# Kernel tuning notes

Measured on AMD Instinct MI355X. Metric: run time of the kernel, lower is better.

## Reference

```python
import jax, jax.numpy as jnp
import numpy as np

B, S, D, DS = 8, 2048, 1024, 128
TEMP = 1.0
C = 8.0


def setup_inputs() -> dict:
    key = jax.random.key(0)
    ks = jax.random.split(key, 8)
    s_in = 1.0 / np.sqrt(D)
    s_st = 1.0 / np.sqrt(DS)
    return {
        "x": jax.random.normal(ks[0], (B, S, D), jnp.float32),
        "W_k": jax.random.normal(ks[1], (DS, D), jnp.float32) * s_in,
        "W_v": jax.random.normal(ks[2], (DS, D), jnp.float32) * s_in,
        "W_q": jax.random.normal(ks[3], (DS, D), jnp.float32) * s_in,
        "W_alpha_w": jax.random.normal(ks[4], (DS, D), jnp.float32) * s_in,
        "W_alpha_b": jnp.zeros((DS,), jnp.float32),
        "lambda_param": jax.random.uniform(ks[5], (DS,), jnp.float32, 4.0, 9.0),
        "W_o": jax.random.normal(ks[6], (D, DS), jnp.float32) * s_st,
        "norm_weight": jnp.ones((DS,), jnp.float32),
    }


def _l2norm(z):
    # matches F.normalize(..., dim=-1) with eps=1e-12
    n = jnp.linalg.norm(z, axis=-1, keepdims=True)
    return z / jnp.maximum(n, 1e-12)


def reference(x, W_k, W_v, W_q, W_alpha_w, W_alpha_b, lambda_param, W_o, norm_weight):
    # projections
    k = _l2norm(x @ W_k.T)                      # [B,S,DS]
    v = x @ W_v.T                               # [B,S,DS]
    q = _l2norm(x @ W_q.T)                      # [B,S,DS]
    r = jax.nn.sigmoid(x @ W_alpha_w.T + W_alpha_b)
    log_a = jnp.log(jax.nn.sigmoid(lambda_param) + 1e-8)  # [DS]
    alpha = jnp.exp(C * r * log_a)              # [B,S,DS], data-dependent decay

    H0 = jnp.zeros((B, DS, DS), x.dtype)        # state indexed [b, k, v]

    def step(H, inp):
        k_t, v_t, q_t, a_t = inp                # each [B,DS]
        # surprise: prediction error against current state
        pred = jnp.einsum('bk,bkv->bv', q_t, H)
        err = jnp.sum((v_t - pred) ** 2, axis=-1, keepdims=True)  # [B,1]
        sur = jax.nn.sigmoid(err / (TEMP + 1e-6))                 # [B,1]
        # delta rule: k (x) v - k (x) (k^T H) = k (x) (v - k^T H)
        k_proj = jnp.einsum('bk,bkv->bv', k_t, H)
        delta = k_t[:, :, None] * (v_t - k_proj)[:, None, :]      # [B,DS,DS]
        a_e = a_t[:, :, None]                                     # decay on k-axis
        H = a_e * H + (1.0 - a_e) * (sur[:, :, None] * delta)
        y = jnp.einsum('bk,bkv->bv', q_t, H)
        return H, y

    seq = (k.transpose(1, 0, 2), v.transpose(1, 0, 2),
           q.transpose(1, 0, 2), alpha.transpose(1, 0, 2))
    _, ys = jax.lax.scan(step, H0, seq)         # ys: [S,B,DS]
    y = ys.transpose(1, 0, 2)                   # [B,S,DS]

    # RMSNorm (computed in fp32, like the torch module)
    yf = y.astype(jnp.float32)
    yn = yf * jax.lax.rsqrt(jnp.mean(yf * yf, axis=-1, keepdims=True) + 1e-6)
    yn = (yn * norm_weight).astype(y.dtype)
    return yn @ W_o.T                           # [B,S,D]
```

## Files before the change

kernel.cpp:

```cpp
#include <hip/hip_runtime.h>
#include <math.h>

#define S_LEN 2048
#define B_SZ 8
#define D_IN 1024
#define DS_ 128
#define INV_TEMP (1.0f/1.000001f)
#define LBUF 712
#define NBLK 16

#define BAR_LDS() asm volatile("s_waitcnt lgkmcnt(0)\n\ts_barrier" ::: "memory")

#define DPPADD(x, ctrl) { int t_ = __builtin_amdgcn_update_dpp( \
    0, __float_as_int(x), ctrl, 0xF, 0xF, false); x += __int_as_float(t_); }
#define ROWSUM(x) { DPPADD(x, 0x128) DPPADD(x, 0x124) DPPADD(x, 0x122) DPPADD(x, 0x121) }

__global__ __launch_bounds__(256) void proj_gemm(
    const float* __restrict__ X,
    const float* __restrict__ Wk, const float* __restrict__ Wv,
    const float* __restrict__ Wq, const float* __restrict__ Wa,
    float* __restrict__ P)
{
    __shared__ __align__(16) float As[32][68];
    __shared__ __align__(16) float Bs[32][68];
    const int tid = threadIdx.x;
    const int m0 = blockIdx.x * 64;
    const int n0 = blockIdx.y * 64;
    const int lr = tid >> 3;
    const int lk4 = tid & 7;

    const float* wrows[2];
#pragma unroll
    for (int i = 0; i < 2; i++) {
        int nn = n0 + lr + i * 32;
        const float* w;
        if      (nn < 128) w = Wk + (size_t)nn * D_IN;
        else if (nn < 256) w = Wv + (size_t)(nn - 128) * D_IN;
        else if (nn < 384) w = Wq + (size_t)(nn - 256) * D_IN;
        else               w = Wa + (size_t)(nn - 384) * D_IN;
        wrows[i] = w;
    }
    const int ty = tid >> 4, tx = tid & 15;
    float acc[4][4];
#pragma unroll
    for (int i = 0; i < 4; i++)
#pragma unroll
        for (int j = 0; j < 4; j++) acc[i][j] = 0.f;

    for (int k0 = 0; k0 < D_IN; k0 += 32) {
#pragma unroll
        for (int i = 0; i < 2; i++) {
            int m = lr + i * 32;
            float4 a4 = *(const float4*)(X + (size_t)(m0 + m) * D_IN + k0 + lk4 * 4);
            As[lk4*4+0][m] = a4.x; As[lk4*4+1][m] = a4.y;
            As[lk4*4+2][m] = a4.z; As[lk4*4+3][m] = a4.w;
            float4 b4 = *(const float4*)(wrows[i] + k0 + lk4 * 4);
            Bs[lk4*4+0][m] = b4.x; Bs[lk4*4+1][m] = b4.y;
            Bs[lk4*4+2][m] = b4.z; Bs[lk4*4+3][m] = b4.w;
        }
        __syncthreads();
#pragma unroll
        for (int kk = 0; kk < 32; kk++) {
            float4 a4 = *(const float4*)(&As[kk][ty * 4]);
            float4 b4 = *(const float4*)(&Bs[kk][tx * 4]);
            float a[4] = {a4.x, a4.y, a4.z, a4.w};
            float b[4] = {b4.x, b4.y, b4.z, b4.w};
#pragma unroll
            for (int i = 0; i < 4; i++)
#pragma unroll
                for (int j = 0; j < 4; j++)
                    acc[i][j] = fmaf(a[i], b[j], acc[i][j]);
        }
        __syncthreads();
    }
#pragma unroll
    for (int i = 0; i < 4; i++) {
        float4 o; o.x = acc[i][0]; o.y = acc[i][1]; o.z = acc[i][2]; o.w = acc[i][3];
        *(float4*)(P + (size_t)(m0 + ty * 4 + i) * 512 + n0 + tx * 4) = o;
    }
}

__global__ __launch_bounds__(128) void postproc(
    float* __restrict__ P, float* __restrict__ G,
    const float* __restrict__ bA, const float* __restrict__ lam)
{
    const int tok = blockIdx.x, i = threadIdx.x;
    float* row = P + (size_t)tok * 512;
    float kr = row[i], qr = row[256 + i], rr = row[384 + i];
    float ks = kr * kr, qs = qr * qr;
#pragma unroll
    for (int m = 1; m < 64; m <<= 1) { ks += __shfl_xor(ks, m); qs += __shfl_xor(qs, m); }
    __shared__ float sb[6];
    if ((i & 63) == 0) { sb[(i >> 6) * 2] = ks; sb[(i >> 6) * 2 + 1] = qs; }
    __syncthreads();
    float kinv = 1.0f / fmaxf(sqrtf(sb[0] + sb[2]), 1e-12f);
    float qinv = 1.0f / fmaxf(sqrtf(sb[1] + sb[3]), 1e-12f);
    float kn = kr * kinv, qn = qr * qinv;
    float sr = 1.0f / (1.0f + __expf(-(rr + bA[i])));
    float sl = 1.0f / (1.0f + __expf(-lam[i]));
    float la = logf(sl + 1e-8f);
    float al = __expf(8.0f * sr * la);
    row[i] = kn; row[256 + i] = qn; row[384 + i] = al;
    float gi = qn * (1.0f - al) * kn;
#pragma unroll
    for (int m = 1; m < 64; m <<= 1) gi += __shfl_xor(gi, m);
    if ((i & 63) == 0) sb[4 + (i >> 6)] = gi;
    __syncthreads();
    if (i == 0) G[tok] = sb[4] + sb[5];
}

__global__ __launch_bounds__(512, 2) void recurrence(
    const float* __restrict__ P, const float* __restrict__ G,
    float* __restrict__ Y, float* __restrict__ EB)
{
    const int bx = blockIdx.x;
    const int b = bx & 7;
    const int half = bx >> 3;
    const int tid = threadIdx.x;
    const int c = tid & 15;
    const int vp = tid >> 4;
    const int lane = tid & 63;
    const int wave = tid >> 6;
    const int co = c * 12;
    const int voff = 576 + half * 64 + vp * 2;

    __shared__ __align__(16) float Pbuf[3][LBUF];
    __shared__ __align__(16) float errw[2][8];

    const float* Pb = P + (size_t)b * S_LEN * 512;
    const float* Gb = G + (size_t)b * S_LEN;
    float* Yb = Y + (size_t)b * S_LEN * DS_ + half * 64;
    float* own = EB + (size_t)bx * S_LEN;
    const float* peer = EB + (size_t)(bx ^ 8) * S_LEN;

    float2 H[8];
#pragma unroll
    for (int j = 0; j < 8; j++) { H[j].x = 0.f; H[j].y = 0.f; }

    const bool isP = tid < 256;
    const bool isG = (tid == 256);
    int spos = 0;
    if (isP) {
        int i = tid * 2, s = i >> 7, idx = i & 127, cp = (idx >> 3) * 12 + (idx & 7);
        spos = (s == 0) ? cp : (s == 1) ? (576 + idx) : (s == 2) ? (192 + cp) : (384 + cp);
    }

    float2 rp0 = {0.f, 0.f}, rp1 = {0.f, 0.f};
    float rg0 = 0.f, rg1 = 0.f;
    if (isP) { rp0 = *(const float2*)(Pb + tid * 2); rp1 = *(const float2*)(Pb + 512 + tid * 2); }
    if (isG) { rg0 = Gb[0]; rg1 = Gb[1]; }
    if (isP) *(float2*)(&Pbuf[0][spos]) = rp0;
    if (isG) Pbuf[0][704] = rg0;
    __syncthreads();

    float4 k0, k1, q0, q1, a0, a1; float2 vt; float g;
#define LOADREGS(T) { float* cb = &Pbuf[(T) % 3][0]; \
    k0 = *(const float4*)(cb + co);       k1 = *(const float4*)(cb + co + 4); \
    q0 = *(const float4*)(cb + 192 + co); q1 = *(const float4*)(cb + 192 + co + 4); \
    a0 = *(const float4*)(cb + 384 + co); a1 = *(const float4*)(cb + 384 + co + 4); \
    vt = *(const float2*)(cb + voff);     g  = cb[704]; }

    LOADREGS(0)

#define STEP(T, PAR, RPS, RGS, RPL, RGL) { \
    float kk[8] = {k0.x,k0.y,k0.z,k0.w,k1.x,k1.y,k1.z,k1.w}; \
    float qq[8] = {q0.x,q0.y,q0.z,q0.w,q1.x,q1.y,q1.z,q1.w}; \
    float aa[8] = {a0.x,a0.y,a0.z,a0.w,a1.x,a1.y,a1.z,a1.w}; \
    float zz[8], ww[8]; \
    _Pragma("unroll") for (int j = 0; j < 8; j++) { \
        zz[j] = qq[j] * aa[j]; ww[j] = fmaf(-kk[j], aa[j], kk[j]); } \
    float2 pr = {0.f,0.f}, kp = {0.f,0.f}, ya = {0.f,0.f}; \
    _Pragma("unroll") for (int j = 0; j < 8; j++) { \
        pr.x = fmaf(qq[j], H[j].x, pr.x); pr.y = fmaf(qq[j], H[j].y, pr.y); \
        kp.x = fmaf(kk[j], H[j].x, kp.x); kp.y = fmaf(kk[j], H[j].y, kp.y); \
        ya.x = fmaf(zz[j], H[j].x, ya.x); ya.y = fmaf(zz[j], H[j].y, ya.y); } \
    ROWSUM(pr.x) ROWSUM(pr.y) ROWSUM(kp.x) ROWSUM(kp.y) ROWSUM(ya.x) ROWSUM(ya.y) \
    float ex = vt.x - pr.x, ey = vt.y - pr.y; \
    float ep = fmaf(ex, ex, ey * ey); \
    ep += __shfl_xor(ep, 16); ep += __shfl_xor(ep, 32); \
    if (lane == 0) errw[PAR][wave] = ep; \
    float2 d2; d2.x = vt.x - kp.x; d2.y = vt.y - kp.y; \
    const float gcur = g; const float2 yac = ya; \
    if ((T) + 1 < S_LEN) { \
        if (isP) *(float2*)(&Pbuf[((T) + 1) % 3][spos]) = RPS; \
        if (isG) Pbuf[((T) + 1) % 3][704] = RGS; } \
    if ((T) + 2 < S_LEN) { \
        if (isP) RPL = *(const float2*)(Pb + (size_t)((T) + 2) * 512 + tid * 2); \
        if (isG) RGL = Gb[(T) + 2]; } \
    BAR_LDS(); \
    const float4 ea  = *(const float4*)(&errw[PAR][0]); \
    const float4 eb2 = *(const float4*)(&errw[PAR][4]); \
    float el = ((ea.x + ea.y) + (ea.z + ea.w)) + ((eb2.x + eb2.y) + (eb2.z + eb2.w)); \
    if (tid == 0) __hip_atomic_store(own + (T), el + 1.0f, \
        __ATOMIC_RELAXED, __HIP_MEMORY_SCOPE_AGENT); \
    _Pragma("unroll") for (int j = 0; j < 8; j++) { H[j].x *= aa[j]; H[j].y *= aa[j]; } \
    if ((T) + 1 < S_LEN) LOADREGS((T) + 1) \
    float pv; \
    do { pv = __hip_atomic_load(peer + (T), \
        __ATOMIC_RELAXED, __HIP_MEMORY_SCOPE_AGENT); } while (pv == 0.0f); \
    float err = el + (pv - 1.0f); \
    float sur = 1.0f / (1.0f + __expf(-err * INV_TEMP)); \
    float2 sd; sd.x = sur * d2.x; sd.y = sur * d2.y; \
    _Pragma("unroll") for (int j = 0; j < 8; j++) { \
        H[j].x = fmaf(ww[j], sd.x, H[j].x); H[j].y = fmaf(ww[j], sd.y, H[j].y); } \
    if (c == 0) { \
        float sg = sur * gcur; float2 y2; \
        y2.x = fmaf(sg, d2.x, yac.x); y2.y = fmaf(sg, d2.y, yac.y); \
        *(float2*)(Yb + (size_t)(T) * DS_ + vp * 2) = y2; } \
}

    for (int t = 0; t < S_LEN; t += 2) {
        STEP(t,     0, rp1, rg1, rp0, rg0)
        STEP(t + 1, 1, rp0, rg0, rp1, rg1)
    }
#undef STEP
#undef LOADREGS
}

__global__ __launch_bounds__(128) void rmsnorm(
    float* __restrict__ Y, const float* __restrict__ nw)
{
    const int tok = blockIdx.x, i = threadIdx.x;
    float y = Y[(size_t)tok * DS_ + i];
    float s = y * y;
#pragma unroll
    for (int m = 1; m < 64; m <<= 1) s += __shfl_xor(s, m);
    __shared__ float sb[2];
    if ((i & 63) == 0) sb[i >> 6] = s;
    __syncthreads();
    float ms = (sb[0] + sb[1]) * (1.0f / 128.0f);
    Y[(size_t)tok * DS_ + i] = y * rsqrtf(ms + 1e-6f) * nw[i];
}

__global__ __launch_bounds__(256) void out_gemm(
    const float* __restrict__ Yn, const float* __restrict__ Wo, float* __restrict__ Out)
{
    __shared__ __align__(16) float As[32][68];
    __shared__ __align__(16) float Bs[32][68];
    const int tid = threadIdx.x;
    const int m0 = blockIdx.x * 64;
    const int n0 = blockIdx.y * 64;
    const int lr = tid >> 3;
    const int lk4 = tid & 7;
    const int ty = tid >> 4, tx = tid & 15;
    float acc[4][4];
#pragma unroll
    for (int i = 0; i < 4; i++)
#pragma unroll
        for (int j = 0; j < 4; j++) acc[i][j] = 0.f;

    for (int k0 = 0; k0 < DS_; k0 += 32) {
#pragma unroll
        for (int i = 0; i < 2; i++) {
            int m = lr + i * 32;
            float4 a4 = *(const float4*)(Yn + (size_t)(m0 + m) * DS_ + k0 + lk4 * 4);
            As[lk4*4+0][m] = a4.x; As[lk4*4+1][m] = a4.y;
            As[lk4*4+2][m] = a4.z; As[lk4*4+3][m] = a4.w;
            float4 b4 = *(const float4*)(Wo + (size_t)(n0 + m) * DS_ + k0 + lk4 * 4);
            Bs[lk4*4+0][m] = b4.x; Bs[lk4*4+1][m] = b4.y;
            Bs[lk4*4+2][m] = b4.z; Bs[lk4*4+3][m] = b4.w;
        }
        __syncthreads();
#pragma unroll
        for (int kk = 0; kk < 32; kk++) {
            float4 a4 = *(const float4*)(&As[kk][ty * 4]);
            float4 b4 = *(const float4*)(&Bs[kk][tx * 4]);
            float a[4] = {a4.x, a4.y, a4.z, a4.w};
            float b[4] = {b4.x, b4.y, b4.z, b4.w};
#pragma unroll
            for (int i = 0; i < 4; i++)
#pragma unroll
                for (int j = 0; j < 4; j++)
                    acc[i][j] = fmaf(a[i], b[j], acc[i][j]);
        }
        __syncthreads();
    }
#pragma unroll
    for (int i = 0; i < 4; i++) {
        float4 o; o.x = acc[i][0]; o.y = acc[i][1]; o.z = acc[i][2]; o.w = acc[i][3];
        *(float4*)(Out + (size_t)(m0 + ty * 4 + i) * 1024 + n0 + tx * 4) = o;
    }
}

extern "C" void kernel_launch(void* const* d_in, const int* in_sizes, int n_in,
                              void* d_out, int out_size, void* d_ws, size_t ws_size,
                              hipStream_t stream)
{
    const float* x   = (const float*)d_in[0];
    const float* Wk  = (const float*)d_in[1];
    const float* Wv  = (const float*)d_in[2];
    const float* Wq  = (const float*)d_in[3];
    const float* Waw = (const float*)d_in[4];
    const float* Wab = (const float*)d_in[5];
    const float* lam = (const float*)d_in[6];
    const float* Wo  = (const float*)d_in[7];
    const float* nw  = (const float*)d_in[8];
    float* out = (float*)d_out;

    const size_t NTOK = (size_t)B_SZ * S_LEN;
    float* P  = (float*)d_ws;
    float* G  = P + NTOK * 512;
    float* Y  = G + NTOK;
    float* EB = Y + NTOK * 128;

    hipMemsetAsync(EB, 0, (size_t)NBLK * S_LEN * sizeof(float), stream);
    proj_gemm<<<dim3(NTOK / 64, 512 / 64), 256, 0, stream>>>(x, Wk, Wv, Wq, Waw, P);
    postproc<<<NTOK, 128, 0, stream>>>(P, G, Wab, lam);
    recurrence<<<NBLK, 512, 0, stream>>>(P, G, Y, EB);
    rmsnorm<<<NTOK, 128, 0, stream>>>(Y, nw);
    out_gemm<<<dim3(NTOK / 64, 1024 / 64), 256, 0, stream>>>(Y, Wo, out);
}
```

Measured before the change: 2.985 ms.

## Run each batch's recurrence in one 1024-thread block, dropping cross-block spin sync

Each batch's recurrence used to be split across two 512-thread blocks that swapped partial surprise errors every step through global-memory atomics and spin-waits. Now a single 1024-thread block holds the whole 128x128 state and reduces the error in LDS, which removes the inter-block handshake, the memset and the G precompute. The output y is now computed directly as q·H after the state update, costing one extra dot-product reduction per step, and the early register prefetch of the next step's k/q/a is dropped. Only 8 blocks run, each with 1024 threads, so each per-step LDS barrier now spans more waves.

Result: no change. 3.028 ms (+1.4%).

```diff
diff --git a/kernel.cpp b/kernel.cpp
--- a/kernel.cpp
+++ b/kernel.cpp
@@ -7,7 +7,6 @@
 #define DS_ 128
 #define INV_TEMP (1.0f/1.000001f)
 #define LBUF 712
-#define NBLK 16
 
 #define BAR_LDS() asm volatile("s_waitcnt lgkmcnt(0)\n\ts_barrier" ::: "memory")
 
@@ -81,7 +80,7 @@
 }
 
 __global__ __launch_bounds__(128) void postproc(
-    float* __restrict__ P, float* __restrict__ G,
+    float* __restrict__ P,
     const float* __restrict__ bA, const float* __restrict__ lam)
 {
     const int tok = blockIdx.x, i = threadIdx.x;
@@ -90,7 +89,7 @@
     float ks = kr * kr, qs = qr * qr;
 #pragma unroll
     for (int m = 1; m < 64; m <<= 1) { ks += __shfl_xor(ks, m); qs += __shfl_xor(qs, m); }
-    __shared__ float sb[6];
+    __shared__ float sb[4];
     if ((i & 63) == 0) { sb[(i >> 6) * 2] = ks; sb[(i >> 6) * 2 + 1] = qs; }
     __syncthreads();
     float kinv = 1.0f / fmaxf(sqrtf(sb[0] + sb[2]), 1e-12f);
@@ -101,44 +100,31 @@
     float la = logf(sl + 1e-8f);
     float al = __expf(8.0f * sr * la);
     row[i] = kn; row[256 + i] = qn; row[384 + i] = al;
-    float gi = qn * (1.0f - al) * kn;
-#pragma unroll
-    for (int m = 1; m < 64; m <<= 1) gi += __shfl_xor(gi, m);
-    if ((i & 63) == 0) sb[4 + (i >> 6)] = gi;
-    __syncthreads();
-    if (i == 0) G[tok] = sb[4] + sb[5];
-}
-
-__global__ __launch_bounds__(512, 2) void recurrence(
-    const float* __restrict__ P, const float* __restrict__ G,
-    float* __restrict__ Y, float* __restrict__ EB)
-{
-    const int bx = blockIdx.x;
-    const int b = bx & 7;
-    const int half = bx >> 3;
+}
+
+__global__ __launch_bounds__(1024, 1) void recurrence(
+    const float* __restrict__ P, float* __restrict__ Y)
+{
+    const int b = blockIdx.x;
     const int tid = threadIdx.x;
     const int c = tid & 15;
     const int vp = tid >> 4;
     const int lane = tid & 63;
     const int wave = tid >> 6;
     const int co = c * 12;
-    const int voff = 576 + half * 64 + vp * 2;
+    const int voff = 576 + vp * 2;
 
     __shared__ __align__(16) float Pbuf[3][LBUF];
-    __shared__ __align__(16) float errw[2][8];
+    __shared__ __align__(16) float errw[2][16];
 
     const float* Pb = P + (size_t)b * S_LEN * 512;
-    const float* Gb = G + (size_t)b * S_LEN;
-    float* Yb = Y + (size_t)b * S_LEN * DS_ + half * 64;
-    float* own = EB + (size_t)bx * S_LEN;
-    const float* peer = EB + (size_t)(bx ^ 8) * S_LEN;
+    float* Yb = Y + (size_t)b * S_LEN * DS_;
 
     float2 H[8];
 #pragma unroll
     for (int j = 0; j < 8; j++) { H[j].x = 0.f; H[j].y = 0.f; }
 
     const bool isP = tid < 256;
-    const bool isG = (tid == 256);
     int spos = 0;
     if (isP) {
         int i = tid * 2, s = i >> 7, idx = i & 127, cp = (idx >> 3) * 12 + (idx & 7);
@@ -146,75 +132,63 @@
     }
 
     float2 rp0 = {0.f, 0.f}, rp1 = {0.f, 0.f};
-    float rg0 = 0.f, rg1 = 0.f;
     if (isP) { rp0 = *(const float2*)(Pb + tid * 2); rp1 = *(const float2*)(Pb + 512 + tid * 2); }
-    if (isG) { rg0 = Gb[0]; rg1 = Gb[1]; }
     if (isP) *(float2*)(&Pbuf[0][spos]) = rp0;
-    if (isG) Pbuf[0][704] = rg0;
     __syncthreads();
 
-    float4 k0, k1, q0, q1, a0, a1; float2 vt; float g;
-#define LOADREGS(T) { float* cb = &Pbuf[(T) % 3][0]; \
-    k0 = *(const float4*)(cb + co);       k1 = *(const float4*)(cb + co + 4); \
-    q0 = *(const float4*)(cb + 192 + co); q1 = *(const float4*)(cb + 192 + co + 4); \
-    a0 = *(const float4*)(cb + 384 + co); a1 = *(const float4*)(cb + 384 + co + 4); \
-    vt = *(const float2*)(cb + voff);     g  = cb[704]; }
-
-    LOADREGS(0)
-
-#define STEP(T, PAR, RPS, RGS, RPL, RGL) { \
+#define STEP(T, PAR, RPS, RPL) { \
+    float* cb = &Pbuf[(T) % 3][0]; \
+    const float4 k0 = *(const float4*)(cb + co); \
+    const float4 k1 = *(const float4*)(cb + co + 4); \
+    const float4 q0 = *(const float4*)(cb + 192 + co); \
+    const float4 q1 = *(const float4*)(cb + 192 + co + 4); \
+    const float4 a0 = *(const float4*)(cb + 384 + co); \
+    const float4 a1 = *(const float4*)(cb + 384 + co + 4); \
+    const float2 vt = *(const float2*)(cb + voff); \
     float kk[8] = {k0.x,k0.y,k0.z,k0.w,k1.x,k1.y,k1.z,k1.w}; \
     float qq[8] = {q0.x,q0.y,q0.z,q0.w,q1.x,q1.y,q1.z,q1.w}; \
     float aa[8] = {a0.x,a0.y,a0.z,a0.w,a1.x,a1.y,a1.z,a1.w}; \
-    float zz[8], ww[8]; \
-    _Pragma("unroll") for (int j = 0; j < 8; j++) { \
-        zz[j] = qq[j] * aa[j]; ww[j] = fmaf(-kk[j], aa[j], kk[j]); } \
-    float2 pr = {0.f,0.f}, kp = {0.f,0.f}, ya = {0.f,0.f}; \
+    float ww[8]; \
+    _Pragma("unroll") for (int j = 0; j < 8; j++) \
+        ww[j] = fmaf(-kk[j], aa[j], kk[j]); \
+    float2 pr = {0.f,0.f}, kp = {0.f,0.f}; \
     _Pragma("unroll") for (int j = 0; j < 8; j++) { \
         pr.x = fmaf(qq[j], H[j].x, pr.x); pr.y = fmaf(qq[j], H[j].y, pr.y); \
-        kp.x = fmaf(kk[j], H[j].x, kp.x); kp.y = fmaf(kk[j], H[j].y, kp.y); \
-        ya.x = fmaf(zz[j], H[j].x, ya.x); ya.y = fmaf(zz[j], H[j].y, ya.y); } \
-    ROWSUM(pr.x) ROWSUM(pr.y) ROWSUM(kp.x) ROWSUM(kp.y) ROWSUM(ya.x) ROWSUM(ya.y) \
+        kp.x = fmaf(kk[j], H[j].x, kp.x); kp.y = fmaf(kk[j], H[j].y, kp.y); } \
+    ROWSUM(pr.x) ROWSUM(pr.y) ROWSUM(kp.x) ROWSUM(kp.y) \
     float ex = vt.x - pr.x, ey = vt.y - pr.y; \
     float ep = fmaf(ex, ex, ey * ey); \
     ep += __shfl_xor(ep, 16); ep += __shfl_xor(ep, 32); \
     if (lane == 0) errw[PAR][wave] = ep; \
     float2 d2; d2.x = vt.x - kp.x; d2.y = vt.y - kp.y; \
-    const float gcur = g; const float2 yac = ya; \
     if ((T) + 1 < S_LEN) { \
-        if (isP) *(float2*)(&Pbuf[((T) + 1) % 3][spos]) = RPS; \
-        if (isG) Pbuf[((T) + 1) % 3][704] = RGS; } \
+        if (isP) *(float2*)(&Pbuf[((T) + 1) % 3][spos]) = RPS; } \
     if ((T) + 2 < S_LEN) { \
-        if (isP) RPL = *(const float2*)(Pb + (size_t)((T) + 2) * 512 + tid * 2); \
-        if (isG) RGL = Gb[(T) + 2]; } \
+        if (isP) RPL = *(const float2*)(Pb + (size_t)((T) + 2) * 512 + tid * 2); } \
     BAR_LDS(); \
-    const float4 ea  = *(const float4*)(&errw[PAR][0]); \
-    const float4 eb2 = *(const float4*)(&errw[PAR][4]); \
-    float el = ((ea.x + ea.y) + (ea.z + ea.w)) + ((eb2.x + eb2.y) + (eb2.z + eb2.w)); \
-    if (tid == 0) __hip_atomic_store(own + (T), el + 1.0f, \
-        __ATOMIC_RELAXED, __HIP_MEMORY_SCOPE_AGENT); \
-    _Pragma("unroll") for (int j = 0; j < 8; j++) { H[j].x *= aa[j]; H[j].y *= aa[j]; } \
-    if ((T) + 1 < S_LEN) LOADREGS((T) + 1) \
-    float pv; \
-    do { pv = __hip_atomic_load(peer + (T), \
-        __ATOMIC_RELAXED, __HIP_MEMORY_SCOPE_AGENT); } while (pv == 0.0f); \
-    float err = el + (pv - 1.0f); \
+    const float4 ea = *(const float4*)(&errw[PAR][0]); \
+    const float4 eb = *(const float4*)(&errw[PAR][4]); \
+    const float4 ec = *(const float4*)(&errw[PAR][8]); \
+    const float4 ed = *(const float4*)(&errw[PAR][12]); \
+    float err = (((ea.x+ea.y)+(ea.z+ea.w)) + ((eb.x+eb.y)+(eb.z+eb.w))) \
+              + (((ec.x+ec.y)+(ec.z+ec.w)) + ((ed.x+ed.y)+(ed.z+ed.w))); \
     float sur = 1.0f / (1.0f + __expf(-err * INV_TEMP)); \
-    float2 sd; sd.x = sur * d2.x; sd.y = sur * d2.y; \
+    float sdx = sur * d2.x, sdy = sur * d2.y; \
     _Pragma("unroll") for (int j = 0; j < 8; j++) { \
-        H[j].x = fmaf(ww[j], sd.x, H[j].x); H[j].y = fmaf(ww[j], sd.y, H[j].y); } \
-    if (c == 0) { \
-        float sg = sur * gcur; float2 y2; \
-        y2.x = fmaf(sg, d2.x, yac.x); y2.y = fmaf(sg, d2.y, yac.y); \
-        *(float2*)(Yb + (size_t)(T) * DS_ + vp * 2) = y2; } \
+        H[j].x = fmaf(aa[j], H[j].x, ww[j] * sdx); \
+        H[j].y = fmaf(aa[j], H[j].y, ww[j] * sdy); } \
+    float2 yo = {0.f,0.f}; \
+    _Pragma("unroll") for (int j = 0; j < 8; j++) { \
+        yo.x = fmaf(qq[j], H[j].x, yo.x); yo.y = fmaf(qq[j], H[j].y, yo.y); } \
+    ROWSUM(yo.x) ROWSUM(yo.y) \
+    if (c == 0) *(float2*)(Yb + (size_t)(T) * DS_ + vp * 2) = yo; \
 }
 
     for (int t = 0; t < S_LEN; t += 2) {
-        STEP(t,     0, rp1, rg1, rp0, rg0)
-        STEP(t + 1, 1, rp0, rg0, rp1, rg1)
+        STEP(t,     0, rp1, rp0)
+        STEP(t + 1, 1, rp0, rp1)
     }
 #undef STEP
-#undef LOADREGS
 }
 
 __global__ __launch_bounds__(128) void rmsnorm(
@@ -299,14 +273,11 @@
 
     const size_t NTOK = (size_t)B_SZ * S_LEN;
     float* P  = (float*)d_ws;
-    float* G  = P + NTOK * 512;
-    float* Y  = G + NTOK;
-    float* EB = Y + NTOK * 128;
-
-    hipMemsetAsync(EB, 0, (size_t)NBLK * S_LEN * sizeof(float), stream);
+    float* Y  = P + NTOK * 512;
+
     proj_gemm<<<dim3(NTOK / 64, 512 / 64), 256, 0, stream>>>(x, Wk, Wv, Wq, Waw, P);
-    postproc<<<NTOK, 128, 0, stream>>>(P, G, Wab, lam);
-    recurrence<<<NBLK, 512, 0, stream>>>(P, G, Y, EB);
+    postproc<<<NTOK, 128, 0, stream>>>(P, Wab, lam);
+    recurrence<<<B_SZ, 1024, 0, stream>>>(P, Y);
     rmsnorm<<<NTOK, 128, 0, stream>>>(Y, nw);
     out_gemm<<<dim3(NTOK / 64, 1024 / 64), 256, 0, stream>>>(Y, Wo, out);
 }
```
